# Performance work log

Measured on AMD Instinct MI355X. Metric: run time of the kernel, lower is better.

The kernel has to match this reference:

```python
import jax, jax.numpy as jnp
import numpy as np

N_GRAPHS = 64  # number of graphs pooled by global_mean_pool


def setup_inputs() -> dict:
    key = jax.random.key(0)
    ks = jax.random.split(key, 10)
    N, E, H, K = 50000, 800000, 128, 3
    x = jax.random.normal(ks[0], (N, H), dtype=jnp.float32)
    edge_index = jax.random.randint(ks[1], (2, E), 0, N)
    edge_weight = jax.random.uniform(ks[2], (E,), dtype=jnp.float32)
    batch = jnp.sort(jax.random.randint(ks[3], (N,), 0, N_GRAPHS))
    # 5 TAGConv layers, each with K+1 = 4 weight matrices [H,H] and one bias [H]
    conv_ws = jax.random.normal(ks[4], (5, K + 1, H, H), dtype=jnp.float32) * 0.05
    conv_bs = jax.random.normal(ks[5], (5, H), dtype=jnp.float32) * 0.01
    lin1_w = jax.random.normal(ks[6], (H, H), dtype=jnp.float32) * 0.05
    lin1_b = jnp.zeros((H,), dtype=jnp.float32)
    lin2_w = jax.random.normal(ks[7], (H, 1), dtype=jnp.float32) * 0.05
    lin2_b = jnp.zeros((1,), dtype=jnp.float32)
    return {"x": x, "edge_index": edge_index, "edge_weight": edge_weight,
            "batch": batch, "conv_ws": conv_ws, "conv_bs": conv_bs,
            "lin1_w": lin1_w, "lin1_b": lin1_b, "lin2_w": lin2_w, "lin2_b": lin2_b}


def _gcn_norm(edge_index, edge_weight, n):
    # TAGConv default: gcn_norm without self-loops
    row, col = edge_index[0], edge_index[1]
    deg = jax.ops.segment_sum(edge_weight, col, num_segments=n)
    deg_safe = jnp.where(deg > 0, deg, 1.0)
    dis = jnp.where(deg > 0, jax.lax.rsqrt(deg_safe), 0.0)
    return dis[row] * edge_weight * dis[col]


def _tagconv(x, w, b, row, col, norm, n):
    # out = sum_k (A_hat^k x) W_k + b
    out = x @ w[0]
    h = x
    for k in range(1, w.shape[0]):
        h = jax.ops.segment_sum(h[row] * norm[:, None], col, num_segments=n)
        out = out + h @ w[k]
    return out + b


def reference(x, edge_index, edge_weight, batch, conv_ws, conv_bs,
              lin1_w, lin1_b, lin2_w, lin2_b):
    n = x.shape[0]
    row, col = edge_index[0], edge_index[1]
    norm = _gcn_norm(edge_index, edge_weight, n)
    h = x
    for i in range(5):
        h = jax.nn.relu(_tagconv(h, conv_ws[i], conv_bs[i], row, col, norm, n))
    # global mean pool per graph (dropout treated as identity / eval mode)
    sums = jax.ops.segment_sum(h, batch, num_segments=N_GRAPHS)
    cnt = jax.ops.segment_sum(jnp.ones((n,), h.dtype), batch, num_segments=N_GRAPHS)
    g = sums / jnp.maximum(cnt, 1.0)[:, None]
    g = g @ lin1_w + lin1_b
    g = g @ lin2_w + lin2_b
    return jax.nn.sigmoid(g)
```

## Files before the change

### kernel.cpp

```cpp
#include <hip/hip_runtime.h>
#include <math.h>

#define H 128
#define NGRAPH 64

using f32x4 = __attribute__((ext_vector_type(4))) float;
using f32x2 = __attribute__((ext_vector_type(2))) float;

__device__ inline float bf2f(ushort u) {
  unsigned int b = ((unsigned int)u) << 16;
  return __builtin_bit_cast(float, b);
}
__device__ inline ushort f2bf(float f) {
  unsigned int u = __builtin_bit_cast(unsigned int, f);
  u = (u + 0x7FFF + ((u >> 16) & 1)) >> 16;
  return (ushort)u;
}

#define ACC8(accv, v, n)                                                                     \
  {                                                                                          \
    f32x2 c;                                                                                 \
    c = __builtin_amdgcn_cvt_pk_f32_fp8((v).x, false);                                       \
    accv[0] = fmaf(n, c[0], accv[0]); accv[1] = fmaf(n, c[1], accv[1]);                      \
    c = __builtin_amdgcn_cvt_pk_f32_fp8((v).x, true);                                        \
    accv[2] = fmaf(n, c[0], accv[2]); accv[3] = fmaf(n, c[1], accv[3]);                      \
    c = __builtin_amdgcn_cvt_pk_f32_fp8((v).y, false);                                       \
    accv[4] = fmaf(n, c[0], accv[4]); accv[5] = fmaf(n, c[1], accv[5]);                      \
    c = __builtin_amdgcn_cvt_pk_f32_fp8((v).y, true);                                        \
    accv[6] = fmaf(n, c[0], accv[6]); accv[7] = fmaf(n, c[1], accv[7]);                      \
  }

__global__ __launch_bounds__(256) void k_cvt_x(const float* __restrict__ x,
                                               unsigned char* __restrict__ x8, int total4) {
  int i = blockIdx.x * blockDim.x + threadIdx.x;
  if (i >= total4) return;
  float4 v = *(const float4*)(x + (size_t)i * 4);
  int p = __builtin_amdgcn_cvt_pk_fp8_f32(v.x, v.y, 0, false);
  p = __builtin_amdgcn_cvt_pk_fp8_f32(v.z, v.w, p, true);
  *(unsigned int*)(x8 + (size_t)i * 4) = (unsigned int)p;
}

__global__ __launch_bounds__(256) void k_cvt_w(const float* __restrict__ w,
                                               unsigned char* __restrict__ w8, int total4) {
  int i = blockIdx.x * blockDim.x + threadIdx.x;
  if (i >= total4) return;
  int f = i * 4;
  int l = f >> 16;
  int j = (f >> 9) & 127;
  int k = f & 511;
  int q = k >> 7, kk = k & 127;
  const float* src = w + (((size_t)(l * 4 + q) * H + kk) * H + j);
  float v0 = src[0], v1 = src[H], v2 = src[2 * H], v3 = src[3 * H];
  int p = __builtin_amdgcn_cvt_pk_fp8_f32(v0, v1, 0, false);
  p = __builtin_amdgcn_cvt_pk_fp8_f32(v2, v3, p, true);
  *(unsigned int*)(w8 + f) = (unsigned int)p;
}

__global__ void k_count(const int* __restrict__ col, int* __restrict__ cnt,
                        int* __restrict__ rank, int E) {
  int e = blockIdx.x * blockDim.x + threadIdx.x;
  if (e < E) rank[e] = atomicAdd(&cnt[col[e]], 1);
}

__global__ __launch_bounds__(256) void k_scan1(const int* __restrict__ cnt,
                                               int* __restrict__ bsum, int N) {
  int i = blockIdx.x * 256 + threadIdx.x;
  int v = (i < N) ? cnt[i] : 0;
  __shared__ int red[256];
  red[threadIdx.x] = v;
  __syncthreads();
  #pragma unroll
  for (int o = 128; o; o >>= 1) {
    if (threadIdx.x < o) red[threadIdx.x] += red[threadIdx.x + o];
    __syncthreads();
  }
  if (threadIdx.x == 0) bsum[blockIdx.x] = red[0];
}

__global__ __launch_bounds__(256) void k_scan2(const int* __restrict__ bsum,
                                               int* __restrict__ boff, int nb) {
  __shared__ int s[256];
  int t = threadIdx.x;
  int v = (t < nb) ? bsum[t] : 0;
  s[t] = v;
  __syncthreads();
  #pragma unroll
  for (int d = 1; d < 256; d <<= 1) {
    int u = (t >= d) ? s[t - d] : 0;
    __syncthreads();
    s[t] += u;
    __syncthreads();
  }
  if (t < nb) boff[t] = s[t] - v;
}

__global__ __launch_bounds__(256) void k_scan3(const int* __restrict__ cnt,
                                               const int* __restrict__ boff,
                                               int* __restrict__ ptr, int N) {
  int t = threadIdx.x;
  int i = blockIdx.x * 256 + t;
  int v = (i < N) ? cnt[i] : 0;
  __shared__ int s[256];
  s[t] = v;
  __syncthreads();
  #pragma unroll
  for (int d = 1; d < 256; d <<= 1) {
    int u = (t >= d) ? s[t - d] : 0;
    __syncthreads();
    s[t] += u;
    __syncthreads();
  }
  int ex = boff[blockIdx.x] + s[t] - v;
  if (i < N) {
    ptr[i] = ex;
    if (i == N - 1) ptr[N] = ex + v;
  }
}

__global__ void k_scatter(const int* __restrict__ row, const int* __restrict__ col,
                          const float* __restrict__ w, const int* __restrict__ ptr,
                          const int* __restrict__ rank, unsigned int* __restrict__ es, int E) {
  int e = blockIdx.x * blockDim.x + threadIdx.x;
  if (e < E) {
    int pos = ptr[col[e]] + rank[e];
    es[pos] = ((unsigned int)row[e] & 0xFFFFu) | ((unsigned int)f2bf(w[e]) << 16);
  }
}

__global__ __launch_bounds__(256) void k_degnorm1(const int* __restrict__ ptr,
                                                  const unsigned int* __restrict__ es,
                                                  float* __restrict__ dis, int N) {
  int v = blockIdx.x * blockDim.x + threadIdx.x;
  if (v >= N) return;
  int s = ptr[v], e = ptr[v + 1];
  float d = 0.f;
  for (int i = s; i < e; i++) d += bf2f((ushort)(es[i] >> 16));
  dis[v] = d > 0.f ? rsqrtf(d) : 0.f;
}

__global__ __launch_bounds__(256) void k_degnorm2(const int* __restrict__ ptr,
                                                  unsigned int* __restrict__ es,
                                                  const float* __restrict__ dis, int N) {
  int v = blockIdx.x * blockDim.x + threadIdx.x;
  if (v >= N) return;
  int s = ptr[v], e = ptr[v + 1];
  float dv = dis[v];
  for (int i = s; i < e; i++) {
    unsigned int u = es[i];
    float nm = dis[u & 0xFFFFu] * bf2f((ushort)(u >> 16)) * dv;
    es[i] = (u & 0xFFFFu) | ((unsigned int)f2bf(nm) << 16);
  }
}

__global__ __launch_bounds__(256) void k_prop(const unsigned char* __restrict__ hin8,
                                              unsigned char* __restrict__ hout8,
                                              const int* __restrict__ ptr,
                                              const unsigned int* __restrict__ es, int N) {
  int node = (blockIdx.x * 256 + threadIdx.x) >> 4;
  if (node >= N) return;
  int l15 = threadIdx.x & 15;
  int s = ptr[node], e = ptr[node + 1];
  float a[8] = {0.f, 0.f, 0.f, 0.f, 0.f, 0.f, 0.f, 0.f};
  float b[8] = {0.f, 0.f, 0.f, 0.f, 0.f, 0.f, 0.f, 0.f};
  const unsigned char* base = hin8 + l15 * 8;
  int i = s;
  for (; i + 3 < e; i += 4) {
    unsigned int u0 = es[i], u1 = es[i + 1], u2 = es[i + 2], u3 = es[i + 3];
    uint2 v0 = *(const uint2*)(base + (size_t)(u0 & 0xFFFFu) * H);
    uint2 v1 = *(const uint2*)(base + (size_t)(u1 & 0xFFFFu) * H);
    uint2 v2 = *(const uint2*)(base + (size_t)(u2 & 0xFFFFu) * H);
    uint2 v3 = *(const uint2*)(base + (size_t)(u3 & 0xFFFFu) * H);
    float n0 = bf2f((ushort)(u0 >> 16));
    float n1 = bf2f((ushort)(u1 >> 16));
    float n2 = bf2f((ushort)(u2 >> 16));
    float n3 = bf2f((ushort)(u3 >> 16));
    ACC8(a, v0, n0);
    ACC8(b, v1, n1);
    ACC8(a, v2, n2);
    ACC8(b, v3, n3);
  }
  for (; i < e; i++) {
    unsigned int u0 = es[i];
    uint2 v0 = *(const uint2*)(base + (size_t)(u0 & 0xFFFFu) * H);
    float n0 = bf2f((ushort)(u0 >> 16));
    ACC8(a, v0, n0);
  }
  #pragma unroll
  for (int j = 0; j < 8; j++) a[j] += b[j];
  int p0 = __builtin_amdgcn_cvt_pk_fp8_f32(a[0], a[1], 0, false);
  p0 = __builtin_amdgcn_cvt_pk_fp8_f32(a[2], a[3], p0, true);
  int p1 = __builtin_amdgcn_cvt_pk_fp8_f32(a[4], a[5], 0, false);
  p1 = __builtin_amdgcn_cvt_pk_fp8_f32(a[6], a[7], p1, true);
  *(uint2*)(hout8 + (size_t)node * H + l15 * 8) = make_uint2((unsigned int)p0, (unsigned int)p1);
}

__global__ __launch_bounds__(256) void k_fgemm(const unsigned char* __restrict__ X0,
                                               const unsigned char* __restrict__ X1,
                                               const unsigned char* __restrict__ X2,
                                               const unsigned char* __restrict__ X3,
                                               const unsigned char* __restrict__ W8,
                                               const float* __restrict__ bias,
                                               unsigned char* __restrict__ O8, int N) {
  __shared__ unsigned char As[128][72];
  __shared__ unsigned char Bs[128][72];
  int t = threadIdx.x;
  int r0 = blockIdx.x * 128;
  int w = t >> 6, lane = t & 63;
  int mw = w >> 1, nw = w & 1;
  int l15 = lane & 15, l4 = lane >> 4;

  f32x4 acc[4][4];
  #pragma unroll
  for (int i = 0; i < 4; i++)
    #pragma unroll
    for (int j = 0; j < 4; j++) acc[i][j] = (f32x4){0.f, 0.f, 0.f, 0.f};

  for (int it = 0; it < 8; ++it) {
    const unsigned char* Xp = (it < 2) ? X0 : (it < 4) ? X1 : (it < 6) ? X2 : X3;
    int kb = (it & 1) * 64;
    int k0 = it * 64;
    #pragma unroll
    for (int p = 0; p < 2; p++) {
      int idx = t + p * 256;
      int rj = idx >> 2;
      int kc = (idx & 3) << 4;
      int gr = r0 + rj;
      uint4 av = make_uint4(0, 0, 0, 0);
      if (gr < N) av = *(const uint4*)(Xp + (size_t)gr * H + kb + kc);
      *(uint4*)&As[rj][kc] = av;
      *(uint4*)&Bs[rj][kc] = *(const uint4*)(W8 + (size_t)rj * 512 + k0 + kc);
    }
    __syncthreads();
    #pragma unroll
    for (int ks = 0; ks < 2; ks++) {
      int kk = ks * 32 + l4 * 8;
      long a[4], b[4];
      #pragma unroll
      for (int mf = 0; mf < 4; mf++) a[mf] = *(const long*)&As[mw * 64 + mf * 16 + l15][kk];
      #pragma unroll
      for (int nf = 0; nf < 4; nf++) b[nf] = *(const long*)&Bs[nw * 64 + nf * 16 + l15][kk];
      #pragma unroll
      for (int mf = 0; mf < 4; mf++)
        #pragma unroll
        for (int nf = 0; nf < 4; nf++)
          acc[mf][nf] = __builtin_amdgcn_mfma_f32_16x16x32_fp8_fp8(a[mf], b[nf], acc[mf][nf], 0, 0, 0);
    }
    __syncthreads();
  }

  #pragma unroll
  for (int nf = 0; nf < 4; nf++) {
    int colj = nw * 64 + nf * 16 + l15;
    float bv = bias[colj];
    #pragma unroll
    for (int mf = 0; mf < 4; mf++) {
      int rbase = r0 + mw * 64 + mf * 16 + l4 * 4;
      #pragma unroll
      for (int r = 0; r < 4; r++) {
        int rr = rbase + r;
        if (rr < N) {
          float v = fmaxf(acc[mf][nf][r] + bv, 0.f);
          O8[(size_t)rr * H + colj] =
              (unsigned char)(__builtin_amdgcn_cvt_pk_fp8_f32(v, v, 0, false) & 0xFF);
        }
      }
    }
  }
}

#define POOL_ROWS 64
__global__ __launch_bounds__(256) void k_pool(const unsigned char* __restrict__ h8,
                                              const int* __restrict__ batch,
                                              float* __restrict__ pooled, int N) {
  int r0 = blockIdx.x * POOL_ROWS;
  int j2 = threadIdx.x & 63;
  int q = threadIdx.x >> 6;
  int rend = min(r0 + POOL_ROWS, N);
  float a0 = 0.f, a1 = 0.f;
  int cur = -1;
  for (int r = r0 + q; r < rend; r += 4) {
    int g = batch[r];
    if (g != cur) {
      if (cur >= 0) {
        atomicAdd(&pooled[cur * H + 2 * j2], a0);
        atomicAdd(&pooled[cur * H + 2 * j2 + 1], a1);
      }
      cur = g;
      a0 = a1 = 0.f;
    }
    unsigned int v = *(const ushort*)(h8 + (size_t)r * H + 2 * j2);
    f32x2 c = __builtin_amdgcn_cvt_pk_f32_fp8(v, false);
    a0 += c[0];
    a1 += c[1];
  }
  if (cur >= 0) {
    atomicAdd(&pooled[cur * H + 2 * j2], a0);
    atomicAdd(&pooled[cur * H + 2 * j2 + 1], a1);
  }
}

__global__ __launch_bounds__(128) void k_head(const float* __restrict__ pooled,
                                              const int* __restrict__ batch, int N,
                                              const float* __restrict__ w1,
                                              const float* __restrict__ b1,
                                              const float* __restrict__ w2,
                                              const float* __restrict__ b2,
                                              float* __restrict__ out) {
  int g = blockIdx.x;
  int j = threadIdx.x;
  __shared__ float pv[H];
  __shared__ float red[H];
  __shared__ int bnd[2];
  if (j < 2) {
    int target = g + j;
    int lo = 0, hi = N;
    while (lo < hi) {
      int mid = (lo + hi) >> 1;
      if (batch[mid] < target) lo = mid + 1;
      else hi = mid;
    }
    bnd[j] = lo;
  }
  __syncthreads();
  float c = (float)max(bnd[1] - bnd[0], 1);
  pv[j] = pooled[g * H + j] / c;
  __syncthreads();
  float t1 = b1[j];
  #pragma unroll 4
  for (int k = 0; k < H; k++) t1 = fmaf(pv[k], w1[k * H + j], t1);
  red[j] = t1 * w2[j];
  __syncthreads();
  if (j < 64) {
    float s = red[j] + red[j + 64];
    #pragma unroll
    for (int o = 32; o; o >>= 1) s += __shfl_down(s, o);
    if (j == 0) out[g] = 1.f / (1.f + expf(-(s + b2[0])));
  }
}

extern "C" void kernel_launch(void* const* d_in, const int* in_sizes, int n_in,
                              void* d_out, int out_size, void* d_ws, size_t ws_size,
                              hipStream_t stream) {
  const float* x = (const float*)d_in[0];
  const int* eidx = (const int*)d_in[1];
  const float* ew = (const float*)d_in[2];
  const int* batch = (const int*)d_in[3];
  const float* conv_ws = (const float*)d_in[4];
  const float* conv_bs = (const float*)d_in[5];
  const float* lin1_w = (const float*)d_in[6];
  const float* lin1_b = (const float*)d_in[7];
  const float* lin2_w = (const float*)d_in[8];
  const float* lin2_b = (const float*)d_in[9];
  float* out = (float*)d_out;

  const int N = in_sizes[0] / H;
  const int E = in_sizes[2];
  const int* row = eidx;
  const int* col = eidx + E;

  char* p = (char*)d_ws;
  auto alloc = [&](size_t bytes) {
    char* q = p;
    p += (bytes + 255) & ~(size_t)255;
    return q;
  };
  int* cnt = (int*)alloc((size_t)N * 4);
  int* ptrb = (int*)alloc((size_t)(N + 1) * 4);
  int* rank = (int*)alloc((size_t)E * 4);
  float* dis = (float*)alloc((size_t)N * 4);
  unsigned int* es = (unsigned int*)alloc((size_t)E * 4);
  unsigned char* x8 = (unsigned char*)alloc((size_t)N * H);
  unsigned char* C0 = (unsigned char*)alloc((size_t)N * H);
  unsigned char* C1 = (unsigned char*)alloc((size_t)N * H);
  unsigned char* C2 = (unsigned char*)alloc((size_t)N * H);
  unsigned char* C3 = (unsigned char*)alloc((size_t)N * H);
  unsigned char* W8 = (unsigned char*)alloc((size_t)5 * H * 512);
  int* bsum = (int*)alloc(256 * 4);
  int* boff = (int*)alloc(256 * 4);
  float* pooled = (float*)alloc((size_t)NGRAPH * H * 4);

  hipMemsetAsync(cnt, 0, (size_t)N * 4, stream);
  hipMemsetAsync(pooled, 0, (size_t)NGRAPH * H * 4, stream);

  int eb = (E + 255) / 256;
  int nb = (N + 255) / 256;
  k_cvt_x<<<(N * H / 4 + 255) / 256, 256, 0, stream>>>(x, x8, N * H / 4);
  k_cvt_w<<<(5 * H * 512 / 4 + 255) / 256, 256, 0, stream>>>(conv_ws, W8, 5 * H * 512 / 4);
  k_count<<<eb, 256, 0, stream>>>(col, cnt, rank, E);
  k_scan1<<<nb, 256, 0, stream>>>(cnt, bsum, N);
  k_scan2<<<1, 256, 0, stream>>>(bsum, boff, nb);
  k_scan3<<<nb, 256, 0, stream>>>(cnt, boff, ptrb, N);
  k_scatter<<<eb, 256, 0, stream>>>(row, col, ew, ptrb, rank, es, E);
  k_degnorm1<<<nb, 256, 0, stream>>>(ptrb, es, dis, N);
  k_degnorm2<<<nb, 256, 0, stream>>>(ptrb, es, dis, N);

  int gemm_blocks = (N + 127) / 128;
  int prop_blocks = (N + 15) / 16;

  const unsigned char* P8 = x8;
  for (int layer = 0; layer < 5; layer++) {
    const unsigned char* Wl = W8 + (size_t)layer * H * 512;
    const float* bl = conv_bs + (size_t)layer * H;
    k_prop<<<prop_blocks, 256, 0, stream>>>(P8, C0, ptrb, es, N);
    k_prop<<<prop_blocks, 256, 0, stream>>>(C0, C1, ptrb, es, N);
    k_prop<<<prop_blocks, 256, 0, stream>>>(C1, C2, ptrb, es, N);
    k_fgemm<<<gemm_blocks, 256, 0, stream>>>(P8, C0, C1, C2, Wl, bl, C3, N);
    P8 = C3;
  }

  k_pool<<<(N + POOL_ROWS - 1) / POOL_ROWS, 256, 0, stream>>>(P8, batch, pooled, N);
  k_head<<<NGRAPH, 128, 0, stream>>>(pooled, batch, N, lin1_w, lin1_b, lin2_w, lin2_b, out);
}
```

Measured before the change: 481.1 us.

## Fuse setup kernels, merge scan passes, unroll prop by 8, fuse pooling into last GEMM

Merges the x/W fp8 conversion and edge counting into one launch, and folds the single-block scan into the per-block scan, with each block summing the preceding block totals itself. The propagation loop is unrolled to 8 gathers in flight and uses nontemporal loads for the edge stream. Global mean pooling is fused into the final layer's GEMM epilogue through shared-memory partial sums plus atomics, which removes the separate pool kernel and the last fp8 store. In exchange it adds shared-memory atomics and register pressure, and pooling now sums unrounded fp32 values instead of fp8-rounded ones.

```diff
diff --git a/kernel.cpp b/kernel.cpp
--- a/kernel.cpp
+++ b/kernel.cpp
@@ -30,36 +30,41 @@
     accv[6] = fmaf(n, c[0], accv[6]); accv[7] = fmaf(n, c[1], accv[7]);                      \
   }
 
-__global__ __launch_bounds__(256) void k_cvt_x(const float* __restrict__ x,
-                                               unsigned char* __restrict__ x8, int total4) {
-  int i = blockIdx.x * blockDim.x + threadIdx.x;
-  if (i >= total4) return;
-  float4 v = *(const float4*)(x + (size_t)i * 4);
-  int p = __builtin_amdgcn_cvt_pk_fp8_f32(v.x, v.y, 0, false);
-  p = __builtin_amdgcn_cvt_pk_fp8_f32(v.z, v.w, p, true);
-  *(unsigned int*)(x8 + (size_t)i * 4) = (unsigned int)p;
-}
-
-__global__ __launch_bounds__(256) void k_cvt_w(const float* __restrict__ w,
-                                               unsigned char* __restrict__ w8, int total4) {
-  int i = blockIdx.x * blockDim.x + threadIdx.x;
-  if (i >= total4) return;
-  int f = i * 4;
-  int l = f >> 16;
-  int j = (f >> 9) & 127;
-  int k = f & 511;
-  int q = k >> 7, kk = k & 127;
-  const float* src = w + (((size_t)(l * 4 + q) * H + kk) * H + j);
-  float v0 = src[0], v1 = src[H], v2 = src[2 * H], v3 = src[3 * H];
-  int p = __builtin_amdgcn_cvt_pk_fp8_f32(v0, v1, 0, false);
-  p = __builtin_amdgcn_cvt_pk_fp8_f32(v2, v3, p, true);
-  *(unsigned int*)(w8 + f) = (unsigned int)p;
-}
-
-__global__ void k_count(const int* __restrict__ col, int* __restrict__ cnt,
-                        int* __restrict__ rank, int E) {
-  int e = blockIdx.x * blockDim.x + threadIdx.x;
-  if (e < E) rank[e] = atomicAdd(&cnt[col[e]], 1);
+__global__ __launch_bounds__(256) void k_setup(const float* __restrict__ x,
+                                               unsigned char* __restrict__ x8,
+                                               const float* __restrict__ w,
+                                               unsigned char* __restrict__ w8,
+                                               const int* __restrict__ col,
+                                               int* __restrict__ cnt, int* __restrict__ rank,
+                                               int nx4, int nw4, int E, int bx, int bw) {
+  int b = blockIdx.x;
+  int t = threadIdx.x;
+  if (b < bx) {
+    int i = b * 256 + t;
+    if (i < nx4) {
+      float4 v = *(const float4*)(x + (size_t)i * 4);
+      int p = __builtin_amdgcn_cvt_pk_fp8_f32(v.x, v.y, 0, false);
+      p = __builtin_amdgcn_cvt_pk_fp8_f32(v.z, v.w, p, true);
+      *(unsigned int*)(x8 + (size_t)i * 4) = (unsigned int)p;
+    }
+  } else if (b < bx + bw) {
+    int i = (b - bx) * 256 + t;
+    if (i < nw4) {
+      int f = i * 4;
+      int l = f >> 16;
+      int j = (f >> 9) & 127;
+      int k = f & 511;
+      int q = k >> 7, kk = k & 127;
+      const float* src = w + (((size_t)(l * 4 + q) * H + kk) * H + j);
+      float v0 = src[0], v1 = src[H], v2 = src[2 * H], v3 = src[3 * H];
+      int p = __builtin_amdgcn_cvt_pk_fp8_f32(v0, v1, 0, false);
+      p = __builtin_amdgcn_cvt_pk_fp8_f32(v2, v3, p, true);
+      *(unsigned int*)(w8 + f) = (unsigned int)p;
+    }
+  } else {
+    int e = (b - bx - bw) * 256 + t;
+    if (e < E) rank[e] = atomicAdd(&cnt[col[e]], 1);
+  }
 }
 
 __global__ __launch_bounds__(256) void k_scan1(const int* __restrict__ cnt,
@@ -77,40 +82,35 @@
   if (threadIdx.x == 0) bsum[blockIdx.x] = red[0];
 }
 
-__global__ __launch_bounds__(256) void k_scan2(const int* __restrict__ bsum,
-                                               int* __restrict__ boff, int nb) {
-  __shared__ int s[256];
+__global__ __launch_bounds__(256) void k_scan3(const int* __restrict__ cnt,
+                                               const int* __restrict__ bsum,
+                                               int* __restrict__ ptr, int N) {
+  int vb = blockIdx.x;
   int t = threadIdx.x;
-  int v = (t < nb) ? bsum[t] : 0;
-  s[t] = v;
+  __shared__ int sh[256];
+  int partial = 0;
+  for (int j = t; j < vb; j += 256) partial += bsum[j];
+  sh[t] = partial;
+  __syncthreads();
+  #pragma unroll
+  for (int o = 128; o; o >>= 1) {
+    if (t < o) sh[t] += sh[t + o];
+    __syncthreads();
+  }
+  int boff = sh[0];
+  __syncthreads();
+  int i = vb * 256 + t;
+  int v = (i < N) ? cnt[i] : 0;
+  sh[t] = v;
   __syncthreads();
   #pragma unroll
   for (int d = 1; d < 256; d <<= 1) {
-    int u = (t >= d) ? s[t - d] : 0;
-    __syncthreads();
-    s[t] += u;
-    __syncthreads();
-  }
-  if (t < nb) boff[t] = s[t] - v;
-}
-
-__global__ __launch_bounds__(256) void k_scan3(const int* __restrict__ cnt,
-                                               const int* __restrict__ boff,
-                                               int* __restrict__ ptr, int N) {
-  int t = threadIdx.x;
-  int i = blockIdx.x * 256 + t;
-  int v = (i < N) ? cnt[i] : 0;
-  __shared__ int s[256];
-  s[t] = v;
-  __syncthreads();
-  #pragma unroll
-  for (int d = 1; d < 256; d <<= 1) {
-    int u = (t >= d) ? s[t - d] : 0;
-    __syncthreads();
-    s[t] += u;
-    __syncthreads();
-  }
-  int ex = boff[blockIdx.x] + s[t] - v;
+    int u = (t >= d) ? sh[t - d] : 0;
+    __syncthreads();
+    sh[t] += u;
+    __syncthreads();
+  }
+  int ex = boff + sh[t] - v;
   if (i < N) {
     ptr[i] = ex;
     if (i == N - 1) ptr[N] = ex + v;
@@ -164,23 +164,35 @@
   float b[8] = {0.f, 0.f, 0.f, 0.f, 0.f, 0.f, 0.f, 0.f};
   const unsigned char* base = hin8 + l15 * 8;
   int i = s;
-  for (; i + 3 < e; i += 4) {
-    unsigned int u0 = es[i], u1 = es[i + 1], u2 = es[i + 2], u3 = es[i + 3];
+  for (; i + 7 < e; i += 8) {
+    unsigned int u[8];
+    #pragma unroll
+    for (int k = 0; k < 8; k++) u[k] = __builtin_nontemporal_load(&es[i + k]);
+    uint2 v[8];
+    #pragma unroll
+    for (int k = 0; k < 8; k++) v[k] = *(const uint2*)(base + (size_t)(u[k] & 0xFFFFu) * H);
+    #pragma unroll
+    for (int k = 0; k < 8; k++) {
+      float n = bf2f((ushort)(u[k] >> 16));
+      if (k & 1) {
+        ACC8(b, v[k], n);
+      } else {
+        ACC8(a, v[k], n);
+      }
+    }
+  }
+  for (; i + 1 < e; i += 2) {
+    unsigned int u0 = __builtin_nontemporal_load(&es[i]);
+    unsigned int u1 = __builtin_nontemporal_load(&es[i + 1]);
     uint2 v0 = *(const uint2*)(base + (size_t)(u0 & 0xFFFFu) * H);
     uint2 v1 = *(const uint2*)(base + (size_t)(u1 & 0xFFFFu) * H);
-    uint2 v2 = *(const uint2*)(base + (size_t)(u2 & 0xFFFFu) * H);
-    uint2 v3 = *(const uint2*)(base + (size_t)(u3 & 0xFFFFu) * H);
     float n0 = bf2f((ushort)(u0 >> 16));
     float n1 = bf2f((ushort)(u1 >> 16));
-    float n2 = bf2f((ushort)(u2 >> 16));
-    float n3 = bf2f((ushort)(u3 >> 16));
     ACC8(a, v0, n0);
     ACC8(b, v1, n1);
-    ACC8(a, v2, n2);
-    ACC8(b, v3, n3);
-  }
-  for (; i < e; i++) {
-    unsigned int u0 = es[i];
+  }
+  if (i < e) {
+    unsigned int u0 = __builtin_nontemporal_load(&es[i]);
     uint2 v0 = *(const uint2*)(base + (size_t)(u0 & 0xFFFFu) * H);
     float n0 = bf2f((ushort)(u0 >> 16));
     ACC8(a, v0, n0);
@@ -194,20 +206,30 @@
   *(uint2*)(hout8 + (size_t)node * H + l15 * 8) = make_uint2((unsigned int)p0, (unsigned int)p1);
 }
 
+template <int LAST>
 __global__ __launch_bounds__(256) void k_fgemm(const unsigned char* __restrict__ X0,
                                                const unsigned char* __restrict__ X1,
                                                const unsigned char* __restrict__ X2,
                                                const unsigned char* __restrict__ X3,
                                                const unsigned char* __restrict__ W8,
                                                const float* __restrict__ bias,
-                                               unsigned char* __restrict__ O8, int N) {
+                                               unsigned char* __restrict__ O8,
+                                               const int* __restrict__ batch,
+                                               float* __restrict__ pooled, int N) {
   __shared__ unsigned char As[128][72];
   __shared__ unsigned char Bs[128][72];
+  __shared__ float pl[4][H];
+  __shared__ int sb[128];
   int t = threadIdx.x;
   int r0 = blockIdx.x * 128;
   int w = t >> 6, lane = t & 63;
   int mw = w >> 1, nw = w & 1;
   int l15 = lane & 15, l4 = lane >> 4;
+
+  if (LAST) {
+    for (int k = t; k < 4 * H; k += 256) ((float*)pl)[k] = 0.f;
+    if (t < 128 && r0 + t < N) sb[t] = batch[r0 + t];
+  }
 
   f32x4 acc[4][4];
   #pragma unroll
@@ -248,54 +270,42 @@
     __syncthreads();
   }
 
+  int g0 = 0;
+  if (LAST) g0 = sb[0];
+
   #pragma unroll
   for (int nf = 0; nf < 4; nf++) {
     int colj = nw * 64 + nf * 16 + l15;
     float bv = bias[colj];
     #pragma unroll
     for (int mf = 0; mf < 4; mf++) {
-      int rbase = r0 + mw * 64 + mf * 16 + l4 * 4;
+      int rbase = mw * 64 + mf * 16 + l4 * 4;
       #pragma unroll
       for (int r = 0; r < 4; r++) {
-        int rr = rbase + r;
+        int rr = r0 + rbase + r;
         if (rr < N) {
           float v = fmaxf(acc[mf][nf][r] + bv, 0.f);
-          O8[(size_t)rr * H + colj] =
-              (unsigned char)(__builtin_amdgcn_cvt_pk_fp8_f32(v, v, 0, false) & 0xFF);
+          if (LAST) {
+            int slot = sb[rbase + r] - g0;
+            if (slot < 4) atomicAdd(&pl[slot][colj], v);
+            else atomicAdd(&pooled[(size_t)sb[rbase + r] * H + colj], v);
+          } else {
+            O8[(size_t)rr * H + colj] =
+                (unsigned char)(__builtin_amdgcn_cvt_pk_fp8_f32(v, v, 0, false) & 0xFF);
+          }
         }
       }
     }
   }
-}
-
-#define POOL_ROWS 64
-__global__ __launch_bounds__(256) void k_pool(const unsigned char* __restrict__ h8,
-                                              const int* __restrict__ batch,
-                                              float* __restrict__ pooled, int N) {
-  int r0 = blockIdx.x * POOL_ROWS;
-  int j2 = threadIdx.x & 63;
-  int q = threadIdx.x >> 6;
-  int rend = min(r0 + POOL_ROWS, N);
-  float a0 = 0.f, a1 = 0.f;
-  int cur = -1;
-  for (int r = r0 + q; r < rend; r += 4) {
-    int g = batch[r];
-    if (g != cur) {
-      if (cur >= 0) {
-        atomicAdd(&pooled[cur * H + 2 * j2], a0);
-        atomicAdd(&pooled[cur * H + 2 * j2 + 1], a1);
-      }
-      cur = g;
-      a0 = a1 = 0.f;
-    }
-    unsigned int v = *(const ushort*)(h8 + (size_t)r * H + 2 * j2);
-    f32x2 c = __builtin_amdgcn_cvt_pk_f32_fp8(v, false);
-    a0 += c[0];
-    a1 += c[1];
-  }
-  if (cur >= 0) {
-    atomicAdd(&pooled[cur * H + 2 * j2], a0);
-    atomicAdd(&pooled[cur * H + 2 * j2 + 1], a1);
+
+  if (LAST) {
+    __syncthreads();
+    for (int k = t; k < 4 * H; k += 256) {
+      int slot = k >> 7, colj = k & 127;
+      float val = pl[slot][colj];
+      if (val != 0.f && g0 + slot < NGRAPH)
+        atomicAdd(&pooled[(size_t)(g0 + slot) * H + colj], val);
+    }
   }
 }
 
@@ -376,21 +386,23 @@
   unsigned char* C3 = (unsigned char*)alloc((size_t)N * H);
   unsigned char* W8 = (unsigned char*)alloc((size_t)5 * H * 512);
   int* bsum = (int*)alloc(256 * 4);
-  int* boff = (int*)alloc(256 * 4);
   float* pooled = (float*)alloc((size_t)NGRAPH * H * 4);
 
   hipMemsetAsync(cnt, 0, (size_t)N * 4, stream);
   hipMemsetAsync(pooled, 0, (size_t)NGRAPH * H * 4, stream);
 
-  int eb = (E + 255) / 256;
+  int nx4 = N * H / 4;
+  int nw4 = 5 * H * 512 / 4;
+  int bx = (nx4 + 255) / 256;
+  int bw = (nw4 + 255) / 256;
+  int be = (E + 255) / 256;
   int nb = (N + 255) / 256;
-  k_cvt_x<<<(N * H / 4 + 255) / 256, 256, 0, stream>>>(x, x8, N * H / 4);
-  k_cvt_w<<<(5 * H * 512 / 4 + 255) / 256, 256, 0, stream>>>(conv_ws, W8, 5 * H * 512 / 4);
-  k_count<<<eb, 256, 0, stream>>>(col, cnt, rank, E);
+
+  k_setup<<<bx + bw + be, 256, 0, stream>>>(x, x8, conv_ws, W8, col, cnt, rank,
+                                            nx4, nw4, E, bx, bw);
   k_scan1<<<nb, 256, 0, stream>>>(cnt, bsum, N);
-  k_scan2<<<1, 256, 0, stream>>>(bsum, boff, nb);
-  k_scan3<<<nb, 256, 0, stream>>>(cnt, boff, ptrb, N);
-  k_scatter<<<eb, 256, 0, stream>>>(row, col, ew, ptrb, rank, es, E);
+  k_scan3<<<nb, 256, 0, stream>>>(cnt, bsum, ptrb, N);
+  k_scatter<<<be, 256, 0, stream>>>(row, col, ew, ptrb, rank, es, E);
   k_degnorm1<<<nb, 256, 0, stream>>>(ptrb, es, dis, N);
   k_degnorm2<<<nb, 256, 0, stream>>>(ptrb, es, dis, N);
 
@@ -404,10 +416,12 @@
     k_prop<<<prop_blocks, 256, 0, stream>>>(P8, C0, ptrb, es, N);
     k_prop<<<prop_blocks, 256, 0, stream>>>(C0, C1, ptrb, es, N);
     k_prop<<<prop_blocks, 256, 0, stream>>>(C1, C2, ptrb, es, N);
-    k_fgemm<<<gemm_blocks, 256, 0, stream>>>(P8, C0, C1, C2, Wl, bl, C3, N);
+    if (layer < 4)
+      k_fgemm<0><<<gemm_blocks, 256, 0, stream>>>(P8, C0, C1, C2, Wl, bl, C3, batch, pooled, N);
+    else
+      k_fgemm<1><<<gemm_blocks, 256, 0, stream>>>(P8, C0, C1, C2, Wl, bl, C3, batch, pooled, N);
     P8 = C3;
   }
 
-  k_pool<<<(N + POOL_ROWS - 1) / POOL_ROWS, 256, 0, stream>>>(P8, batch, pooled, N);
   k_head<<<NGRAPH, 128, 0, stream>>>(pooled, batch, N, lin1_w, lin1_b, lin2_w, lin2_b, out);
 }
```

Result: slower. 545.5 us (+13.4%).
